# Performance work log

Hardware: AMD Instinct MI355X
Metric: run time of the kernel (lower is better)

Reference implementation:

```python
import math
import jax, jax.numpy as jnp
import numpy as np

H = 1024        # hidden_size
NH = 16         # num_attention_heads
HD = H // NH    # attention_head_size
I = 4096        # intermediate_size
B, S = 4, 2048
LN_EPS = 1e-5


def setup_inputs() -> dict:
    key = jax.random.key(0)
    ks = jax.random.split(key, 12)
    s = 0.02
    return {
        "x": jax.random.normal(ks[0], (B, S, H), dtype=jnp.float32),
        "ln1_g": jnp.ones((H,), jnp.float32),
        "ln1_b": jnp.zeros((H,), jnp.float32),
        "qkv_w": jax.random.normal(ks[1], (H, 3 * H), jnp.float32) * s,
        "qkv_b": jnp.zeros((3 * H,), jnp.float32),
        "out_w": jax.random.normal(ks[2], (H, H), jnp.float32) * s,
        "out_b": jnp.zeros((H,), jnp.float32),
        "ln2_g": jnp.ones((H,), jnp.float32),
        "ln2_b": jnp.zeros((H,), jnp.float32),
        "w1": jax.random.normal(ks[3], (H, I), jnp.float32) * s,
        "b1": jnp.zeros((I,), jnp.float32),
        "w2": jax.random.normal(ks[4], (I, H), jnp.float32) * s,
        "b2": jnp.zeros((H,), jnp.float32),
    }


def _layernorm(x, g, b):
    mu = jnp.mean(x, axis=-1, keepdims=True)
    var = jnp.mean(jnp.square(x - mu), axis=-1, keepdims=True)
    return (x - mu) * jax.lax.rsqrt(var + LN_EPS) * g + b


def _gelu_tanh(x):
    c = math.sqrt(2.0 / math.pi)
    return 0.5 * x * (1.0 + jnp.tanh(c * (x + 0.044715 * x * x * x)))


def reference(x, ln1_g, ln1_b, qkv_w, qkv_b, out_w, out_b, ln2_g, ln2_b, w1, b1, w2, b2):
    b, s, _ = x.shape
    h = _layernorm(x, ln1_g, ln1_b)
    qkv = h @ qkv_w + qkv_b                      # [B,S,3H]
    q, k, v = jnp.split(qkv, 3, axis=-1)
    # [B,S,H] -> [B,NH,S,HD]
    def heads(t):
        return t.reshape(b, s, NH, HD).transpose(0, 2, 1, 3)
    q, k, v = heads(q), heads(k), heads(v)
    scores = jnp.einsum("bhqd,bhkd->bhqk", q, k) / math.sqrt(HD)
    probs = jax.nn.softmax(scores, axis=-1)
    attn = jnp.einsum("bhqk,bhkd->bhqd", probs, v)
    attn = attn.transpose(0, 2, 1, 3).reshape(b, s, H)
    attn = attn @ out_w + out_b
    x = x + attn
    h2 = _layernorm(x, ln2_g, ln2_b)
    mlp = _gelu_tanh(h2 @ w1 + b1) @ w2 + b2
    x = x + mlp
    return x
```

## Files before the change

kernel.cpp:

```cpp
#include <hip/hip_runtime.h>
#include <math.h>

#define H 1024
#define NHEAD 16
#define HDIM 64
#define IDIM 4096
#define BATCH 4
#define SEQ 2048
#define NTOK 8192
#define LN_EPS 1e-5f

#define QK_EXP2_SCALE 0.18033688011112042f

typedef __bf16 bf16x8 __attribute__((ext_vector_type(8)));
typedef __bf16 bf16x4 __attribute__((ext_vector_type(4)));
typedef float f32x4 __attribute__((ext_vector_type(4)));
typedef unsigned short ushort8 __attribute__((ext_vector_type(8)));
typedef unsigned short ushort4v __attribute__((ext_vector_type(4)));

__device__ __forceinline__ unsigned short f2bf(float f) {
  union { float f; unsigned int u; } v; v.f = f;
  unsigned int u = v.u;
  return (unsigned short)((u + 0x7FFFu + ((u >> 16) & 1u)) >> 16);
}

__global__ void transpose_cast_kernel(const float* __restrict__ W,
                                      unsigned short* __restrict__ Wt,
                                      int K, int N) {
  __shared__ unsigned short tile[32][33];
  int n0 = blockIdx.x * 32, k0 = blockIdx.y * 32;
  int tx = threadIdx.x, ty = threadIdx.y;
#pragma unroll
  for (int i = 0; i < 4; i++) {
    int k = ty + i * 8;
    tile[tx][k] = f2bf(W[(size_t)(k0 + k) * N + n0 + tx]);
  }
  __syncthreads();
#pragma unroll
  for (int i = 0; i < 4; i++) {
    int n = ty + i * 8;
    Wt[(size_t)(n0 + n) * K + k0 + tx] = tile[n][tx];
  }
}

__global__ __launch_bounds__(256)
void layernorm_kernel(const float* __restrict__ x, const float* __restrict__ g,
                      const float* __restrict__ b, unsigned short* __restrict__ out) {
  __shared__ float sb[4];
  int row = blockIdx.x;
  int tid = threadIdx.x;
  const float4* xr = (const float4*)(x + (size_t)row * H);
  float4 v = xr[tid];
  float s = v.x + v.y + v.z + v.w;
#pragma unroll
  for (int o = 32; o > 0; o >>= 1) s += __shfl_down(s, o);
  if ((tid & 63) == 0) sb[tid >> 6] = s;
  __syncthreads();
  float mu = (sb[0] + sb[1] + sb[2] + sb[3]) * (1.0f / H);
  __syncthreads();
  float dx = v.x - mu, dy = v.y - mu, dz = v.z - mu, dw = v.w - mu;
  float s2 = dx * dx + dy * dy + dz * dz + dw * dw;
#pragma unroll
  for (int o = 32; o > 0; o >>= 1) s2 += __shfl_down(s2, o);
  if ((tid & 63) == 0) sb[tid >> 6] = s2;
  __syncthreads();
  float var = (sb[0] + sb[1] + sb[2] + sb[3]) * (1.0f / H);
  float rs = rsqrtf(var + LN_EPS);
  float4 gv = ((const float4*)g)[tid];
  float4 bv = ((const float4*)b)[tid];
  ushort4v ov;
  ov[0] = f2bf(dx * rs * gv.x + bv.x);
  ov[1] = f2bf(dy * rs * gv.y + bv.y);
  ov[2] = f2bf(dz * rs * gv.z + bv.z);
  ov[3] = f2bf(dw * rs * gv.w + bv.w);
  ((ushort4v*)(out + (size_t)row * H))[tid] = ov;
}

template <int EPI>
__global__ __launch_bounds__(256)
void gemm_bt_kernel(const unsigned short* __restrict__ A,
                    const unsigned short* __restrict__ Bt,
                    const float* __restrict__ bias,
                    const float* __restrict__ res,
                    void* __restrict__ out, unsigned short* __restrict__ vt_out,
                    int M, int N, int K) {
  __shared__ __align__(16) unsigned short As[2][128 * 32];
  __shared__ __align__(16) unsigned short Bs[2][128 * 32];
  int tid = threadIdx.x;
  int wave = tid >> 6, lane = tid & 63;
  int quad = lane >> 4, l16 = lane & 15;
  int wm = wave >> 1, wn = wave & 1;
  int m0 = blockIdx.y * 128, n0 = blockIdx.x * 128;
  f32x4 acc[4][4];
#pragma unroll
  for (int i = 0; i < 4; i++)
#pragma unroll
    for (int j = 0; j < 4; j++) acc[i][j] = (f32x4){0.f, 0.f, 0.f, 0.f};

  int rl = (lane >> 2);
  int cphys = lane & 3;

  auto stage = [&](int k0, int sel) {
#pragma unroll
    for (int t = 0; t < 2; t++) {
      int ch = wave * 2 + t;
      int rloc = ch * 16 + rl;
      int clog = cphys ^ ((rloc >> 1) & 3);
      const unsigned short* ga = A + (size_t)(m0 + rloc) * K + k0 + clog * 8;
      __builtin_amdgcn_global_load_lds(
          (const __attribute__((address_space(1))) unsigned int*)ga,
          (__attribute__((address_space(3))) unsigned int*)(&As[sel][ch * 512]), 16, 0, 0);
      const unsigned short* gb = Bt + (size_t)(n0 + rloc) * K + k0 + clog * 8;
      __builtin_amdgcn_global_load_lds(
          (const __attribute__((address_space(1))) unsigned int*)gb,
          (__attribute__((address_space(3))) unsigned int*)(&Bs[sel][ch * 512]), 16, 0, 0);
    }
  };

  stage(0, 0);
  for (int k0 = 0; k0 < K; k0 += 32) {
    int sel = (k0 >> 5) & 1;
    __syncthreads();
    if (k0 + 32 < K) stage(k0 + 32, sel ^ 1);
    bf16x8 af[4], bfv[4];
#pragma unroll
    for (int i = 0; i < 4; i++) {
      int ra = wm * 64 + i * 16 + l16;
      af[i] = *(const bf16x8*)&As[sel][ra * 32 + ((quad ^ ((ra >> 1) & 3)) << 3)];
      int rb = wn * 64 + i * 16 + l16;
      bfv[i] = *(const bf16x8*)&Bs[sel][rb * 32 + ((quad ^ ((rb >> 1) & 3)) << 3)];
    }
#pragma unroll
    for (int i = 0; i < 4; i++)
#pragma unroll
      for (int j = 0; j < 4; j++)
        acc[i][j] = __builtin_amdgcn_mfma_f32_16x16x32_bf16(bfv[j], af[i], acc[i][j], 0, 0, 0);
  }
  bool vslice = (EPI == 0) && (vt_out != nullptr) && (n0 >= 2 * H);
#pragma unroll
  for (int i = 0; i < 4; i++) {
    int m = m0 + wm * 64 + i * 16 + l16;
#pragma unroll
    for (int j = 0; j < 4; j++) {
      int nb = n0 + wn * 64 + j * 16 + quad * 4;
      float4 bv4 = *(const float4*)&bias[nb];
      float v0 = acc[i][j][0] + bv4.x;
      float v1 = acc[i][j][1] + bv4.y;
      float v2 = acc[i][j][2] + bv4.z;
      float v3 = acc[i][j][3] + bv4.w;
      size_t off = (size_t)m * N + nb;
      if (EPI == 0) {
        if (vslice) {
          int bb = m >> 11, s = m & (SEQ - 1);
          int cb = nb - 2 * H;
          int hh = cb >> 6, dd = cb & 63;
          size_t base = ((size_t)(bb * NHEAD + hh) * HDIM + dd) * SEQ + s;
          vt_out[base] = f2bf(v0);
          vt_out[base + SEQ] = f2bf(v1);
          vt_out[base + 2 * SEQ] = f2bf(v2);
          vt_out[base + 3 * SEQ] = f2bf(v3);
        } else {
          if (n0 < H) {
            v0 *= QK_EXP2_SCALE; v1 *= QK_EXP2_SCALE;
            v2 *= QK_EXP2_SCALE; v3 *= QK_EXP2_SCALE;
          }
          bf16x4 pk = {(__bf16)v0, (__bf16)v1, (__bf16)v2, (__bf16)v3};
          *(bf16x4*)&((unsigned short*)out)[off] = pk;
        }
      } else if (EPI == 1) {
        float g0 = v0 / (1.f + __expf(-1.5957691216057308f * (v0 + 0.044715f * v0 * v0 * v0)));
        float g1 = v1 / (1.f + __expf(-1.5957691216057308f * (v1 + 0.044715f * v1 * v1 * v1)));
        float g2 = v2 / (1.f + __expf(-1.5957691216057308f * (v2 + 0.044715f * v2 * v2 * v2)));
        float g3 = v3 / (1.f + __expf(-1.5957691216057308f * (v3 + 0.044715f * v3 * v3 * v3)));
        bf16x4 pk = {(__bf16)g0, (__bf16)g1, (__bf16)g2, (__bf16)g3};
        *(bf16x4*)&((unsigned short*)out)[off] = pk;
      } else {
        float4 rv = *(const float4*)&res[off];
        float4 o4;
        o4.x = v0 + rv.x; o4.y = v1 + rv.y; o4.z = v2 + rv.z; o4.w = v3 + rv.w;
        *(float4*)&((float*)out)[off] = o4;
      }
    }
  }
}

__global__ __launch_bounds__(256)
void flash_attn_kernel(const unsigned short* __restrict__ qkv,
                       const unsigned short* __restrict__ vt,
                       unsigned short* __restrict__ attn_out) {
  constexpr int LPs = 40;
  __shared__ __align__(16) unsigned short Ks[2][64 * 64];
  __shared__ __align__(16) unsigned short Ps[4 * 32 * LPs];
  int tid = threadIdx.x;
  int wave = tid >> 6, lane = tid & 63;
  int quad = lane >> 4, l16 = lane & 15;
  int d = blockIdx.x;
  int logical = (d & 7) * 128 + (d >> 3);
  int bh = logical >> 4, qi = logical & 15;
  int b = bh >> 4, h = bh & 15;
  int qblk = qi * 128 + wave * 32;
  const size_t qrow = 3 * H;
  const size_t tok0 = (size_t)b * SEQ;
  const size_t vbase = (size_t)bh * HDIM * SEQ;
  unsigned short* Psw = Ps + wave * 32 * LPs;

  bf16x8 qb[2][2];
#pragma unroll
  for (int mb = 0; mb < 2; mb++)
#pragma unroll
    for (int ks = 0; ks < 2; ks++)
      qb[mb][ks] = *(const bf16x8*)&qkv[(tok0 + qblk + mb * 16 + l16) * qrow +
                                        h * HDIM + ks * 32 + quad * 8];

  float l_part[2] = {0.f, 0.f};
  f32x4 o_acc[2][4];
#pragma unroll
  for (int mb = 0; mb < 2; mb++)
#pragma unroll
    for (int db = 0; db < 4; db++) o_acc[mb][db] = (f32x4){0.f, 0.f, 0.f, 0.f};

  int srow = lane >> 3;
  int schunk = (lane & 7) ^ srow;

#pragma unroll
  for (int t = 0; t < 2; t++) {
    int rbase = wave * 16 + t * 8;
    const unsigned short* ga =
        &qkv[(tok0 + rbase + srow) * qrow + H + h * HDIM + schunk * 8];
    __builtin_amdgcn_global_load_lds(
        (const __attribute__((address_space(1))) unsigned int*)ga,
        (__attribute__((address_space(3))) unsigned int*)(&Ks[0][rbase * 64]), 16, 0, 0);
  }

  for (int kv0 = 0; kv0 < SEQ; kv0 += 64) {
    int buf = (kv0 >> 6) & 1;
    const unsigned short* Kb = Ks[buf];
    unsigned short* Kn = Ks[buf ^ 1];
    __syncthreads();
    bf16x8 va[4][2];
#pragma unroll
    for (int db = 0; db < 4; db++)
#pragma unroll
      for (int ks = 0; ks < 2; ks++)
        va[db][ks] = *(const bf16x8*)&vt[vbase + (size_t)(db * 16 + l16) * SEQ +
                                         kv0 + ks * 32 + quad * 8];
    if (kv0 + 64 < SEQ) {
#pragma unroll
      for (int t = 0; t < 2; t++) {
        int rbase = wave * 16 + t * 8;
        const unsigned short* ga =
            &qkv[(tok0 + kv0 + 64 + rbase + srow) * qrow + H + h * HDIM + schunk * 8];
        __builtin_amdgcn_global_load_lds(
            (const __attribute__((address_space(1))) unsigned int*)ga,
            (__attribute__((address_space(3))) unsigned int*)(Kn + rbase * 64), 16, 0, 0);
      }
    }
#pragma unroll
    for (int half = 0; half < 2; half++) {
#pragma unroll
      for (int nbl = 0; nbl < 2; nbl++) {
        int nb = half * 2 + nbl;
        int row = nb * 16 + l16;
        bf16x8 ka[2];
#pragma unroll
        for (int ks = 0; ks < 2; ks++) {
          int pc = (ks * 4 + quad) ^ (row & 7);
          ka[ks] = *(const bf16x8*)&Kb[row * 64 + pc * 8];
        }
        f32x4 st[2];
#pragma unroll
        for (int mb = 0; mb < 2; mb++) st[mb] = (f32x4){0.f, 0.f, 0.f, 0.f};
        __builtin_amdgcn_s_setprio(1);
#pragma unroll
        for (int ks = 0; ks < 2; ks++)
#pragma unroll
          for (int mb = 0; mb < 2; mb++)
            st[mb] = __builtin_amdgcn_mfma_f32_16x16x32_bf16(ka[ks], qb[mb][ks], st[mb], 0, 0, 0);
        __builtin_amdgcn_s_setprio(0);
#pragma unroll
        for (int mb = 0; mb < 2; mb++) {
          float p0, p1, p2, p3;
          asm("v_exp_f32 %0, %1" : "=v"(p0) : "v"(st[mb][0]));
          asm("v_exp_f32 %0, %1" : "=v"(p1) : "v"(st[mb][1]));
          asm("v_exp_f32 %0, %1" : "=v"(p2) : "v"(st[mb][2]));
          asm("v_exp_f32 %0, %1" : "=v"(p3) : "v"(st[mb][3]));
          l_part[mb] += (p0 + p1) + (p2 + p3);
          bf16x4 pk = {(__bf16)p0, (__bf16)p1, (__bf16)p2, (__bf16)p3};
          *(bf16x4*)&Psw[(mb * 16 + l16) * LPs + nb * 16 + quad * 4] = pk;
        }
      }
      __asm__ volatile("s_waitcnt lgkmcnt(0)" ::: "memory");
      bf16x8 pb[2];
#pragma unroll
      for (int mb = 0; mb < 2; mb++)
        pb[mb] = *(const bf16x8*)&Psw[(mb * 16 + l16) * LPs + half * 32 + quad * 8];
      __builtin_amdgcn_s_setprio(1);
#pragma unroll
      for (int db = 0; db < 4; db++)
#pragma unroll
        for (int mb = 0; mb < 2; mb++)
          o_acc[mb][db] = __builtin_amdgcn_mfma_f32_16x16x32_bf16(va[db][half], pb[mb],
                                                                  o_acc[mb][db], 0, 0, 0);
      __builtin_amdgcn_s_setprio(0);
    }
  }
#pragma unroll
  for (int mb = 0; mb < 2; mb++) {
    l_part[mb] += __shfl_xor(l_part[mb], 16);
    l_part[mb] += __shfl_xor(l_part[mb], 32);
    l_part[mb] = 1.0f / l_part[mb];
  }
#pragma unroll
  for (int mb = 0; mb < 2; mb++) {
#pragma unroll
    for (int db = 0; db < 4; db++) {
      ushort4v o;
#pragma unroll
      for (int r = 0; r < 4; r++) o[r] = f2bf(o_acc[mb][db][r] * l_part[mb]);
      *(ushort4v*)&attn_out[(tok0 + qblk + mb * 16 + l16) * H + h * HDIM +
                            db * 16 + quad * 4] = o;
    }
  }
}

extern "C" void kernel_launch(void* const* d_in, const int* in_sizes, int n_in,
                              void* d_out, int out_size, void* d_ws, size_t ws_size,
                              hipStream_t stream) {
  const float* x = (const float*)d_in[0];
  const float* ln1_g = (const float*)d_in[1];
  const float* ln1_b = (const float*)d_in[2];
  const float* qkv_w = (const float*)d_in[3];
  const float* qkv_b = (const float*)d_in[4];
  const float* out_w = (const float*)d_in[5];
  const float* out_b = (const float*)d_in[6];
  const float* ln2_g = (const float*)d_in[7];
  const float* ln2_b = (const float*)d_in[8];
  const float* w1 = (const float*)d_in[9];
  const float* b1 = (const float*)d_in[10];
  const float* w2 = (const float*)d_in[11];
  const float* b2 = (const float*)d_in[12];
  float* outp = (float*)d_out;

  size_t off = 0;
  auto take = [&](size_t n) {
    char* p = (char*)d_ws + off;
    off += (n + 255) & ~(size_t)255;
    return p;
  };
  unsigned short* h1 = (unsigned short*)take((size_t)NTOK * H * 2);
  unsigned short* qkvb = (unsigned short*)take((size_t)NTOK * 3 * H * 2);
  unsigned short* attn = (unsigned short*)take((size_t)NTOK * H * 2);
  float* x1 = (float*)take((size_t)NTOK * H * 4);
  unsigned short* qkvwt = (unsigned short*)take((size_t)3 * H * H * 2);
  unsigned short* outwt = (unsigned short*)take((size_t)H * H * 2);
  unsigned short* w1t = (unsigned short*)take((size_t)H * IDIM * 2);
  unsigned short* w2t = (unsigned short*)take((size_t)H * IDIM * 2);
  unsigned short* h2 = h1;
  unsigned short* mid = qkvb;
  unsigned short* vt = (unsigned short*)x1;

  dim3 tb(32, 8);
  transpose_cast_kernel<<<dim3(3 * H / 32, H / 32), tb, 0, stream>>>(qkv_w, qkvwt, H, 3 * H);
  transpose_cast_kernel<<<dim3(H / 32, H / 32), tb, 0, stream>>>(out_w, outwt, H, H);
  transpose_cast_kernel<<<dim3(IDIM / 32, H / 32), tb, 0, stream>>>(w1, w1t, H, IDIM);
  transpose_cast_kernel<<<dim3(H / 32, IDIM / 32), tb, 0, stream>>>(w2, w2t, IDIM, H);

  layernorm_kernel<<<NTOK, 256, 0, stream>>>(x, ln1_g, ln1_b, h1);
  gemm_bt_kernel<0><<<dim3(3 * H / 128, NTOK / 128), 256, 0, stream>>>(
      h1, qkvwt, qkv_b, nullptr, qkvb, vt, NTOK, 3 * H, H);
  flash_attn_kernel<<<dim3(SEQ / 128 * BATCH * NHEAD), 256, 0, stream>>>(qkvb, vt, attn);
  gemm_bt_kernel<2><<<dim3(H / 128, NTOK / 128), 256, 0, stream>>>(
      attn, outwt, out_b, x, x1, nullptr, NTOK, H, H);
  layernorm_kernel<<<NTOK, 256, 0, stream>>>(x1, ln2_g, ln2_b, h2);
  gemm_bt_kernel<1><<<dim3(IDIM / 128, NTOK / 128), 256, 0, stream>>>(
      h2, w1t, b1, nullptr, mid, nullptr, NTOK, IDIM, H);
  gemm_bt_kernel<2><<<dim3(H / 128, NTOK / 128), 256, 0, stream>>>(
      mid, w2t, b2, x1, outp, nullptr, NTOK, H, IDIM);
}
```

Measured before the change: 628.1 us.

## Use 512-thread attention blocks covering 256 queries and split V loads per half

Result: faster. 611.3 us (-2.7%).

```diff
diff --git a/kernel.cpp b/kernel.cpp
--- a/kernel.cpp
+++ b/kernel.cpp
@@ -184,21 +184,21 @@
   }
 }
 
-__global__ __launch_bounds__(256)
+__global__ __launch_bounds__(512, 4)
 void flash_attn_kernel(const unsigned short* __restrict__ qkv,
                        const unsigned short* __restrict__ vt,
                        unsigned short* __restrict__ attn_out) {
   constexpr int LPs = 40;
   __shared__ __align__(16) unsigned short Ks[2][64 * 64];
-  __shared__ __align__(16) unsigned short Ps[4 * 32 * LPs];
+  __shared__ __align__(16) unsigned short Ps[8 * 32 * LPs];
   int tid = threadIdx.x;
   int wave = tid >> 6, lane = tid & 63;
   int quad = lane >> 4, l16 = lane & 15;
   int d = blockIdx.x;
-  int logical = (d & 7) * 128 + (d >> 3);
-  int bh = logical >> 4, qi = logical & 15;
+  int logical = (d & 7) * 64 + (d >> 3);
+  int bh = logical >> 3, qi = logical & 7;
   int b = bh >> 4, h = bh & 15;
-  int qblk = qi * 128 + wave * 32;
+  int qblk = qi * 256 + wave * 32;
   const size_t qrow = 3 * H;
   const size_t tok0 = (size_t)b * SEQ;
   const size_t vbase = (size_t)bh * HDIM * SEQ;
@@ -222,14 +222,12 @@
   int srow = lane >> 3;
   int schunk = (lane & 7) ^ srow;
 
-#pragma unroll
-  for (int t = 0; t < 2; t++) {
-    int rbase = wave * 16 + t * 8;
+  {
     const unsigned short* ga =
-        &qkv[(tok0 + rbase + srow) * qrow + H + h * HDIM + schunk * 8];
+        &qkv[(tok0 + wave * 8 + srow) * qrow + H + h * HDIM + schunk * 8];
     __builtin_amdgcn_global_load_lds(
         (const __attribute__((address_space(1))) unsigned int*)ga,
-        (__attribute__((address_space(3))) unsigned int*)(&Ks[0][rbase * 64]), 16, 0, 0);
+        (__attribute__((address_space(3))) unsigned int*)(&Ks[0][wave * 8 * 64]), 16, 0, 0);
   }
 
   for (int kv0 = 0; kv0 < SEQ; kv0 += 64) {
@@ -237,23 +235,17 @@
     const unsigned short* Kb = Ks[buf];
     unsigned short* Kn = Ks[buf ^ 1];
     __syncthreads();
-    bf16x8 va[4][2];
+    bf16x8 va[4];
 #pragma unroll
     for (int db = 0; db < 4; db++)
-#pragma unroll
-      for (int ks = 0; ks < 2; ks++)
-        va[db][ks] = *(const bf16x8*)&vt[vbase + (size_t)(db * 16 + l16) * SEQ +
-                                         kv0 + ks * 32 + quad * 8];
+      va[db] = *(const bf16x8*)&vt[vbase + (size_t)(db * 16 + l16) * SEQ +
+                                   kv0 + quad * 8];
     if (kv0 + 64 < SEQ) {
-#pragma unroll
-      for (int t = 0; t < 2; t++) {
-        int rbase = wave * 16 + t * 8;
-        const unsigned short* ga =
-            &qkv[(tok0 + kv0 + 64 + rbase + srow) * qrow + H + h * HDIM + schunk * 8];
-        __builtin_amdgcn_global_load_lds(
-            (const __attribute__((address_space(1))) unsigned int*)ga,
-            (__attribute__((address_space(3))) unsigned int*)(Kn + rbase * 64), 16, 0, 0);
-      }
+      const unsigned short* ga =
+          &qkv[(tok0 + kv0 + 64 + wave * 8 + srow) * qrow + H + h * HDIM + schunk * 8];
+      __builtin_amdgcn_global_load_lds(
+          (const __attribute__((address_space(1))) unsigned int*)ga,
+          (__attribute__((address_space(3))) unsigned int*)(Kn + wave * 8 * 64), 16, 0, 0);
     }
 #pragma unroll
     for (int half = 0; half < 2; half++) {
@@ -299,9 +291,15 @@
       for (int db = 0; db < 4; db++)
 #pragma unroll
         for (int mb = 0; mb < 2; mb++)
-          o_acc[mb][db] = __builtin_amdgcn_mfma_f32_16x16x32_bf16(va[db][half], pb[mb],
+          o_acc[mb][db] = __builtin_amdgcn_mfma_f32_16x16x32_bf16(va[db], pb[mb],
                                                                   o_acc[mb][db], 0, 0, 0);
       __builtin_amdgcn_s_setprio(0);
+      if (half == 0) {
+#pragma unroll
+        for (int db = 0; db < 4; db++)
+          va[db] = *(const bf16x8*)&vt[vbase + (size_t)(db * 16 + l16) * SEQ +
+                                       kv0 + 32 + quad * 8];
+      }
     }
   }
 #pragma unroll
@@ -368,7 +366,7 @@
   layernorm_kernel<<<NTOK, 256, 0, stream>>>(x, ln1_g, ln1_b, h1);
   gemm_bt_kernel<0><<<dim3(3 * H / 128, NTOK / 128), 256, 0, stream>>>(
       h1, qkvwt, qkv_b, nullptr, qkvb, vt, NTOK, 3 * H, H);
-  flash_attn_kernel<<<dim3(SEQ / 128 * BATCH * NHEAD), 256, 0, stream>>>(qkvb, vt, attn);
+  flash_attn_kernel<<<dim3(SEQ / 256 * BATCH * NHEAD), 512, 0, stream>>>(qkvb, vt, attn);
   gemm_bt_kernel<2><<<dim3(H / 128, NTOK / 128), 256, 0, stream>>>(
       attn, outwt, out_b, x, x1, nullptr, NTOK, H, H);
   layernorm_kernel<<<NTOK, 256, 0, stream>>>(x1, ln2_g, ln2_b, h2);
```
